# Kernel optimization log

Measured on AMD Instinct MI355X. Metric: run time of the kernel, lower is better.

## Reference

```python
import jax, jax.numpy as jnp
import numpy as np
import math

NUM_HEADS = 16
HEAD_DIM = 64
D_MODEL = NUM_HEADS * HEAD_DIM  # 1024
B, S = 4, 2048

def setup_inputs() -> dict:
    key = jax.random.key(0)
    ks = jax.random.split(key, 8)
    sd = 1.0 / math.sqrt(D_MODEL)
    return {
        "hidden_states": jax.random.normal(ks[0], (B, S, D_MODEL), jnp.float32),
        "attention_mask": jnp.zeros((B, 1, 1, S), jnp.float32),
        "Wq": jax.random.normal(ks[1], (D_MODEL, D_MODEL), jnp.float32) * sd,
        "bq": jnp.zeros((D_MODEL,), jnp.float32),
        "Wk": jax.random.normal(ks[2], (D_MODEL, D_MODEL), jnp.float32) * sd,
        "bk": jnp.zeros((D_MODEL,), jnp.float32),
        "Wv": jax.random.normal(ks[3], (D_MODEL, D_MODEL), jnp.float32) * sd,
        "bv": jnp.zeros((D_MODEL,), jnp.float32),
    }

def _split_heads(x):
    # [B, S, D] -> [B, H, S, hd]
    b, s, _ = x.shape
    return x.reshape(b, s, NUM_HEADS, HEAD_DIM).transpose(0, 2, 1, 3)

def reference(hidden_states, attention_mask, Wq, bq, Wk, bk, Wv, bv):
    # Linear projections (torch nn.Linear: x @ W.T + b)
    q = _split_heads(hidden_states @ Wq.T + bq)
    k = _split_heads(hidden_states @ Wk.T + bk)
    v = _split_heads(hidden_states @ Wv.T + bv)
    scale = 1.0 / math.sqrt(HEAD_DIM)
    # [B, H, Sq, Sk] attention scores, fully materialized as in the original
    scores = jnp.einsum("bhqd,bhkd->bhqk", q, k) * scale + attention_mask
    # relusq replacement for softmax
    probs = jnp.square(jax.nn.relu(scores))
    ctx = jnp.einsum("bhqk,bhkd->bhqd", probs, v)  # [B, H, S, hd]
    b = ctx.shape[0]
    return ctx.transpose(0, 2, 1, 3).reshape(b, -1, D_MODEL)
```

## Files before the change

### kernel.cpp

```cpp
#include <hip/hip_runtime.h>


typedef __bf16 bf16x8 __attribute__((ext_vector_type(8)));
typedef __bf16 bf16x4 __attribute__((ext_vector_type(4)));
typedef __bf16 bf16x2 __attribute__((ext_vector_type(2)));
typedef short  s16x4  __attribute__((ext_vector_type(4)));
typedef float  f32x4  __attribute__((ext_vector_type(4)));
typedef float  f32x16 __attribute__((ext_vector_type(16)));
typedef float  floatx4 __attribute__((ext_vector_type(4)));
typedef unsigned u32x2 __attribute__((ext_vector_type(2)));
typedef unsigned u32x4 __attribute__((ext_vector_type(4)));

#define MFMA16(a, b, c) __builtin_amdgcn_mfma_f32_16x16x32_bf16(a, b, c, 0, 0, 0)
#define MFMA32(a, b, c) __builtin_amdgcn_mfma_f32_32x32x16_bf16(a, b, c, 0, 0, 0)

#define WAITCNT_VM0() __builtin_amdgcn_s_waitcnt(0x0F70)
#define WAITCNT_VM6() __builtin_amdgcn_s_waitcnt(0x0F76)
#define BARRIER() __builtin_amdgcn_s_barrier()
#define SETPRIO(p) __builtin_amdgcn_s_setprio(p)

__device__ __forceinline__ void glds16(const __bf16* g, __bf16* l) {
    __builtin_amdgcn_global_load_lds(
        (const __attribute__((address_space(1))) void*)g,
        (__attribute__((address_space(3))) void*)l, 16, 0, 0);
}

__global__ __launch_bounds__(256) void convert_kernel(
    const float* __restrict__ X, const float* __restrict__ Wq,
    const float* __restrict__ Wk, const float* __restrict__ Wv,
    __bf16* __restrict__ Xb, __bf16* __restrict__ Wqb,
    __bf16* __restrict__ Wkb, __bf16* __restrict__ Wvb)
{
    int blk = blockIdx.x;
    const float* src; __bf16* dst; size_t base;
    if (blk < 4096)      { src = X;  dst = Xb;  base = (size_t)blk * 2048; }
    else if (blk < 4608) { src = Wq; dst = Wqb; base = (size_t)(blk - 4096) * 2048; }
    else if (blk < 5120) { src = Wk; dst = Wkb; base = (size_t)(blk - 4608) * 2048; }
    else                 { src = Wv; dst = Wvb; base = (size_t)(blk - 5120) * 2048; }
    size_t off = base + (size_t)threadIdx.x * 8;
    floatx4 a = *(const floatx4*)(src + off);
    floatx4 c = *(const floatx4*)(src + off + 4);
    bf16x8 o;
    o[0] = (__bf16)a[0]; o[1] = (__bf16)a[1]; o[2] = (__bf16)a[2]; o[3] = (__bf16)a[3];
    o[4] = (__bf16)c[0]; o[5] = (__bf16)c[1]; o[6] = (__bf16)c[2]; o[7] = (__bf16)c[3];
    *(bf16x8*)(dst + off) = o;
}

__global__ __launch_bounds__(512, 2) void qkv_gemm_kernel(
    const __bf16* __restrict__ Xb,
    const __bf16* __restrict__ Wqb, const __bf16* __restrict__ Wkb,
    const __bf16* __restrict__ Wvb,
    const float* __restrict__ bq, const float* __restrict__ bk,
    const float* __restrict__ bv,
    __bf16* __restrict__ qws, __bf16* __restrict__ kws, __bf16* __restrict__ vws)
{
    __shared__ __bf16 As[3][256 * 64];
    __shared__ __bf16 Bs[3][128 * 64];

    const int tid  = threadIdx.x;
    const int lane = tid & 63;
    const int wave = tid >> 6;
    const int quad = lane >> 4;
    const int l16  = lane & 15;
    const int m0   = blockIdx.y * 256;

    const int sel = blockIdx.x >> 3;
    const bool vmode = (sel == 2);
    const __bf16* Wb = (sel == 0) ? Wqb : (sel == 1) ? Wkb : Wvb;
    const float* bias = (sel == 0) ? bq : (sel == 1) ? bk : bv;
    __bf16* outp = (sel == 0) ? qws : (sel == 1) ? kws : vws;
    const int n0 = (blockIdx.x & 7) * 128;

    const int wA = vmode ? (wave & 3) * 64 : (wave >> 2) * 64;
    const int wB = vmode ? (wave >> 2) * 64 : (wave & 3) * 64;

    const int srow = lane >> 3;
    const int schk = lane & 7;

    f32x4 acc[4][4] = {};

#define QKV_STAGE_A(bb, kt, i) { \
        int rb_ = wave * 32 + (i) * 8; int r_ = rb_ + srow; \
        int c_ = schk ^ (r_ & 7); \
        glds16(Xb + (size_t)(m0 + r_) * 1024 + (kt) * 64 + c_ * 8, \
               &As[bb][rb_ * 64]); }
#define QKV_STAGE_B(bb, kt, i) { \
        int rb_ = wave * 16 + (i) * 8; int r_ = rb_ + srow; \
        int c_ = schk ^ (r_ & 7); \
        glds16(Wb + (size_t)(n0 + r_) * 1024 + (kt) * 64 + c_ * 8, \
               &Bs[bb][rb_ * 64]); }

    #pragma unroll
    for (int i = 0; i < 4; ++i) QKV_STAGE_A(0, 0, i);
    #pragma unroll
    for (int i = 0; i < 2; ++i) QKV_STAGE_B(0, 0, i);
    #pragma unroll
    for (int i = 0; i < 4; ++i) QKV_STAGE_A(1, 1, i);
    #pragma unroll
    for (int i = 0; i < 2; ++i) QKV_STAGE_B(1, 1, i);
    WAITCNT_VM6();
    BARRIER();

    for (int s = 0; s < 16; ++s) {
        const int cb  = s % 3;
        const int pb  = (s + 2) % 3;
        const int kt2 = (s + 2) & 15;
        const __bf16* Pa_ = vmode ? &As[cb][0] : &Bs[cb][0];
        const __bf16* Pb_ = vmode ? &Bs[cb][0] : &As[cb][0];

        #pragma unroll
        for (int p = 0; p < 2; ++p) {
            bf16x8 af[4], bfr[4];
            #pragma unroll
            for (int a = 0; a < 4; ++a)
                af[a] = *(const bf16x8*)&Pa_[(wA + a * 16 + l16) * 64 +
                                             (((p * 4 + quad) ^ (l16 & 7)) * 8)];
            #pragma unroll
            for (int bb = 0; bb < 4; ++bb)
                bfr[bb] = *(const bf16x8*)&Pb_[(wB + bb * 16 + l16) * 64 +
                                               (((p * 4 + quad) ^ (l16 & 7)) * 8)];
            QKV_STAGE_A(pb, kt2, 2 * p);
            QKV_STAGE_A(pb, kt2, 2 * p + 1);
            QKV_STAGE_B(pb, kt2, p);

            if (p == 1) WAITCNT_VM6();
            BARRIER();

            SETPRIO(1);
            #pragma unroll
            for (int a = 0; a < 4; ++a)
                #pragma unroll
                for (int bb = 0; bb < 4; ++bb)
                    acc[a][bb] = MFMA16(af[a], bfr[bb], acc[a][bb]);
            SETPRIO(0);
            BARRIER();
        }
    }

#undef QKV_STAGE_A
#undef QKV_STAGE_B

    if (!vmode) {
        #pragma unroll
        for (int a = 0; a < 4; ++a) {
            int n = n0 + wA + a * 16 + quad * 4;
            floatx4 bv4 = *(const floatx4*)&bias[n];
            int h = n >> 6, d0 = n & 63;
            #pragma unroll
            for (int bb = 0; bb < 4; ++bb) {
                int m = m0 + wB + bb * 16 + l16;
                int bt = m >> 11, ss = m & 2047;
                bf16x4 o;
                #pragma unroll
                for (int r = 0; r < 4; ++r)
                    o[r] = (__bf16)(acc[a][bb][r] + bv4[r]);
                *(bf16x4*)&outp[((size_t)(bt * 16 + h) * 2048 + ss) * 64 + d0] = o;
            }
        }
    } else {
        #pragma unroll
        for (int a = 0; a < 4; ++a) {
            int m = m0 + wA + a * 16 + quad * 4;
            int bt = m >> 11, s0 = m & 2047;
            #pragma unroll
            for (int bb = 0; bb < 4; ++bb) {
                int n = n0 + wB + bb * 16 + l16;
                float bvv = bias[n];
                int h = n >> 6, d = n & 63;
                bf16x4 o;
                #pragma unroll
                for (int r = 0; r < 4; ++r)
                    o[r] = (__bf16)(acc[a][bb][r] + bvv);
                *(bf16x4*)&outp[((size_t)(bt * 16 + h) * 64 + d) * 2048 + s0] = o;
            }
        }
    }
}

__global__ __launch_bounds__(512, 4) void attn_kernel(
    const __bf16* __restrict__ Q, const __bf16* __restrict__ K,
    const __bf16* __restrict__ Vt, const float* __restrict__ mask,
    float* __restrict__ out)
{
    __shared__ __bf16 Ks[2][2][64 * 64];
    __shared__ __bf16 Vs[2][2][64 * 64];
    __shared__ float  Ms[2048];

    const int tid  = threadIdx.x;
    const int lane = tid & 63;
    const int wave = tid >> 6;
    const int l32  = lane & 31;
    const int hi   = lane >> 5;
    const int bh   = blockIdx.x;
    const int b    = bh >> 4;
    const int h    = bh & 15;
    const int q0w  = blockIdx.y * 256 + wave * 32;

    const __bf16* Qb = Q  + (size_t)bh * 2048 * 64;
    const __bf16* Kb = K  + (size_t)bh * 2048 * 64;
    const __bf16* Vb = Vt + (size_t)bh * 64 * 2048;
    const float*  mb = mask + b * 2048;

    const int rb = wave * 8;
    const int sr = rb + (lane >> 3);
    const int sc = ((lane & 7) ^ (sr & 7)) * 8;

    bf16x8 aq[4];
    #pragma unroll
    for (int dk = 0; dk < 4; ++dk)
        aq[dk] = *(const bf16x8*)(Qb +
            (size_t)(q0w + l32) * 64 + dk * 16 + hi * 8);

    f32x16 co0 = {}, co1 = {};

    glds16(Kb + (size_t)sr * 64 + sc,        &Ks[0][0][rb * 64]);
    glds16(Kb + (size_t)(64 + sr) * 64 + sc, &Ks[0][1][rb * 64]);
    glds16(Vb + (size_t)sr * 2048 + sc,      &Vs[0][0][rb * 64]);
    glds16(Vb + (size_t)sr * 2048 + 64 + sc, &Vs[0][1][rb * 64]);
    glds16((const __bf16*)mb + (size_t)wave * 512 + lane * 8,
           (__bf16*)Ms + wave * 512);
    WAITCNT_VM0();
    BARRIER();

    for (int t = 0; t < 16; ++t) {
        const int kn = ((t + 1) & 15) * 128;
        const int nb = (t + 1) & 1;
        const int cb = t & 1;
        glds16(Kb + (size_t)(kn + sr) * 64 + sc,       &Ks[nb][0][rb * 64]);
        glds16(Kb + (size_t)(kn + 64 + sr) * 64 + sc,  &Ks[nb][1][rb * 64]);
        glds16(Vb + (size_t)sr * 2048 + kn + sc,       &Vs[nb][0][rb * 64]);
        glds16(Vb + (size_t)sr * 2048 + kn + 64 + sc,  &Vs[nb][1][rb * 64]);

        #pragma unroll
        for (int hf = 0; hf < 2; ++hf) {
            const __bf16* Kt = &Ks[cb][hf][0];
            const __bf16* Vtl = &Vs[cb][hf][0];
            const int k0 = t * 128 + hf * 64;

            f32x16 st0 = {}, st1 = {};
            SETPRIO(1);
            #pragma unroll
            for (int dk = 0; dk < 4; ++dk) {
                const int g = dk * 2 + hi;
                const int c0 = (g ^ (l32 & 7)) * 8;
                bf16x8 ak0 = *(const bf16x8*)&Kt[l32 * 64 + c0];
                bf16x8 ak1 = *(const bf16x8*)&Kt[(32 + l32) * 64 + c0];
                st0 = MFMA32(ak0, aq[dk], st0);
                st1 = MFMA32(ak1, aq[dk], st1);
            }
            SETPRIO(0);

            #pragma unroll
            for (int kg = 0; kg < 2; ++kg) {
                const f32x16 s = kg ? st1 : st0;
                const f32x4 zero4 = {};
                unsigned W[4][2];
                #pragma unroll
                for (int G = 0; G < 4; ++G) {
                    f32x4 v;
                    v[0] = s[G * 4 + 0]; v[1] = s[G * 4 + 1];
                    v[2] = s[G * 4 + 2]; v[3] = s[G * 4 + 3];
                    f32x4 mk = *(const f32x4*)&Ms[k0 + kg * 32 + G * 8 + hi * 4];
                    v = v * 0.125f + mk;
                    v = __builtin_elementwise_max(v, zero4);
                    v = v * v;
                    bf16x2 w0, w1;
                    w0[0] = (__bf16)v[0]; w0[1] = (__bf16)v[1];
                    w1[0] = (__bf16)v[2]; w1[1] = (__bf16)v[3];
                    W[G][0] = __builtin_bit_cast(unsigned, w0);
                    W[G][1] = __builtin_bit_cast(unsigned, w1);
                }
                u32x2 s00 = __builtin_amdgcn_permlane32_swap(W[0][0], W[1][0], false, false);
                u32x2 s01 = __builtin_amdgcn_permlane32_swap(W[0][1], W[1][1], false, false);
                u32x2 s10 = __builtin_amdgcn_permlane32_swap(W[2][0], W[3][0], false, false);
                u32x2 s11 = __builtin_amdgcn_permlane32_swap(W[2][1], W[3][1], false, false);
                u32x4 f0, f1;
                f0[0] = s00[0]; f0[1] = s01[0]; f0[2] = s00[1]; f0[3] = s01[1];
                f1[0] = s10[0]; f1[1] = s11[0]; f1[2] = s10[1]; f1[3] = s11[1];
                bf16x8 pa0 = __builtin_bit_cast(bf16x8, f0);
                bf16x8 pa1 = __builtin_bit_cast(bf16x8, f1);

                SETPRIO(1);
                #pragma unroll
                for (int dt = 0; dt < 2; ++dt) {
                    const int d = dt * 32 + l32;
                    const int ch0 = (kg * 4 + hi) ^ (d & 7);
                    const int ch1 = (kg * 4 + 2 + hi) ^ (d & 7);
                    bf16x8 vb0 = *(const bf16x8*)&Vtl[d * 64 + ch0 * 8];
                    bf16x8 vb1 = *(const bf16x8*)&Vtl[d * 64 + ch1 * 8];
                    if (dt == 0) {
                        co0 = MFMA32(pa0, vb0, co0);
                        co0 = MFMA32(pa1, vb1, co0);
                    } else {
                        co1 = MFMA32(pa0, vb0, co1);
                        co1 = MFMA32(pa1, vb1, co1);
                    }
                }
                SETPRIO(0);
            }
        }

        WAITCNT_VM0();
        BARRIER();
    }

    #pragma unroll
    for (int r = 0; r < 16; ++r) {
        int q = q0w + (r & 3) + 8 * (r >> 2) + 4 * hi;
        float* orow = &out[(((size_t)b * 2048 + q) * 16 + h) * 64];
        orow[l32]      = co0[r];
        orow[32 + l32] = co1[r];
    }
}

extern "C" void kernel_launch(void* const* d_in, const int* in_sizes, int n_in,
                              void* d_out, int out_size, void* d_ws, size_t ws_size,
                              hipStream_t stream) {
    const float* hidden = (const float*)d_in[0];
    const float* mask   = (const float*)d_in[1];
    const float* Wq     = (const float*)d_in[2];
    const float* bq     = (const float*)d_in[3];
    const float* Wk     = (const float*)d_in[4];
    const float* bk     = (const float*)d_in[5];
    const float* Wv     = (const float*)d_in[6];
    const float* bv     = (const float*)d_in[7];
    float* out = (float*)d_out;

    __bf16* qws = (__bf16*)d_ws;
    __bf16* kws = qws + (size_t)64 * 2048 * 64;
    __bf16* vws = kws + (size_t)64 * 2048 * 64;
    __bf16* Xb  = vws + (size_t)64 * 2048 * 64;
    __bf16* Wqb = Xb  + (size_t)8192 * 1024;
    __bf16* Wkb = Wqb + (size_t)1024 * 1024;
    __bf16* Wvb = Wkb + (size_t)1024 * 1024;

    convert_kernel<<<dim3(5632), dim3(256), 0, stream>>>(hidden, Wq, Wk, Wv,
                                                         Xb, Wqb, Wkb, Wvb);
    qkv_gemm_kernel<<<dim3(24, 32), dim3(512), 0, stream>>>(Xb, Wqb, Wkb, Wvb,
                                                            bq, bk, bv,
                                                            qws, kws, vws);
    attn_kernel<<<dim3(64, 8), dim3(512), 0, stream>>>(qws, kws, vws, mask, out);
}
```

Baseline: 240.9 us.

## Give each attention wave two 32-row query tiles, halving waves per block

The attention kernel now runs 4 waves of 256 threads per block, each owning 64 query rows as two 32-row groups. K and V fragments read from LDS are reused across both query groups, which halves LDS read traffic per MFMA. Each thread loads twice as many K/V/mask chunks per stage. The cost is roughly double the accumulator and fragment registers, with launch bounds relaxed to 2 blocks per SM. Fewer waves are then available to hide latency.

```diff
diff --git a/kernel.cpp b/kernel.cpp
--- a/kernel.cpp
+++ b/kernel.cpp
@@ -177,7 +177,7 @@
     }
 }
 
-__global__ __launch_bounds__(512, 4) void attn_kernel(
+__global__ __launch_bounds__(256, 2) void attn_kernel(
     const __bf16* __restrict__ Q, const __bf16* __restrict__ K,
     const __bf16* __restrict__ Vt, const float* __restrict__ mask,
     float* __restrict__ out)
@@ -194,31 +194,39 @@
     const int bh   = blockIdx.x;
     const int b    = bh >> 4;
     const int h    = bh & 15;
-    const int q0w  = blockIdx.y * 256 + wave * 32;
+    const int q0w  = blockIdx.y * 256 + wave * 64;
 
     const __bf16* Qb = Q  + (size_t)bh * 2048 * 64;
     const __bf16* Kb = K  + (size_t)bh * 2048 * 64;
     const __bf16* Vb = Vt + (size_t)bh * 64 * 2048;
     const float*  mb = mask + b * 2048;
 
-    const int rb = wave * 8;
+    const int rb = wave * 16;
     const int sr = rb + (lane >> 3);
     const int sc = ((lane & 7) ^ (sr & 7)) * 8;
 
-    bf16x8 aq[4];
-    #pragma unroll
-    for (int dk = 0; dk < 4; ++dk)
-        aq[dk] = *(const bf16x8*)(Qb +
-            (size_t)(q0w + l32) * 64 + dk * 16 + hi * 8);
-
-    f32x16 co0 = {}, co1 = {};
-
-    glds16(Kb + (size_t)sr * 64 + sc,        &Ks[0][0][rb * 64]);
-    glds16(Kb + (size_t)(64 + sr) * 64 + sc, &Ks[0][1][rb * 64]);
-    glds16(Vb + (size_t)sr * 2048 + sc,      &Vs[0][0][rb * 64]);
-    glds16(Vb + (size_t)sr * 2048 + 64 + sc, &Vs[0][1][rb * 64]);
-    glds16((const __bf16*)mb + (size_t)wave * 512 + lane * 8,
-           (__bf16*)Ms + wave * 512);
+    bf16x8 aq[2][4];
+    #pragma unroll
+    for (int qg = 0; qg < 2; ++qg)
+        #pragma unroll
+        for (int dk = 0; dk < 4; ++dk)
+            aq[qg][dk] = *(const bf16x8*)(Qb +
+                (size_t)(q0w + qg * 32 + l32) * 64 + dk * 16 + hi * 8);
+
+    f32x16 co[2][2] = {};
+
+    glds16(Kb + (size_t)sr * 64 + sc,              &Ks[0][0][rb * 64]);
+    glds16(Kb + (size_t)(sr + 8) * 64 + sc,        &Ks[0][0][(rb + 8) * 64]);
+    glds16(Kb + (size_t)(64 + sr) * 64 + sc,       &Ks[0][1][rb * 64]);
+    glds16(Kb + (size_t)(64 + sr + 8) * 64 + sc,   &Ks[0][1][(rb + 8) * 64]);
+    glds16(Vb + (size_t)sr * 2048 + sc,            &Vs[0][0][rb * 64]);
+    glds16(Vb + (size_t)(sr + 8) * 2048 + sc,      &Vs[0][0][(rb + 8) * 64]);
+    glds16(Vb + (size_t)sr * 2048 + 64 + sc,       &Vs[0][1][rb * 64]);
+    glds16(Vb + (size_t)(sr + 8) * 2048 + 64 + sc, &Vs[0][1][(rb + 8) * 64]);
+    glds16((const __bf16*)mb + (size_t)(wave * 2) * 512 + lane * 8,
+           (__bf16*)Ms + (wave * 2) * 512);
+    glds16((const __bf16*)mb + (size_t)(wave * 2 + 1) * 512 + lane * 8,
+           (__bf16*)Ms + (wave * 2 + 1) * 512);
     WAITCNT_VM0();
     BARRIER();
 
@@ -226,10 +234,14 @@
         const int kn = ((t + 1) & 15) * 128;
         const int nb = (t + 1) & 1;
         const int cb = t & 1;
-        glds16(Kb + (size_t)(kn + sr) * 64 + sc,       &Ks[nb][0][rb * 64]);
-        glds16(Kb + (size_t)(kn + 64 + sr) * 64 + sc,  &Ks[nb][1][rb * 64]);
-        glds16(Vb + (size_t)sr * 2048 + kn + sc,       &Vs[nb][0][rb * 64]);
-        glds16(Vb + (size_t)sr * 2048 + kn + 64 + sc,  &Vs[nb][1][rb * 64]);
+        glds16(Kb + (size_t)(kn + sr) * 64 + sc,            &Ks[nb][0][rb * 64]);
+        glds16(Kb + (size_t)(kn + sr + 8) * 64 + sc,        &Ks[nb][0][(rb + 8) * 64]);
+        glds16(Kb + (size_t)(kn + 64 + sr) * 64 + sc,       &Ks[nb][1][rb * 64]);
+        glds16(Kb + (size_t)(kn + 64 + sr + 8) * 64 + sc,   &Ks[nb][1][(rb + 8) * 64]);
+        glds16(Vb + (size_t)sr * 2048 + kn + sc,            &Vs[nb][0][rb * 64]);
+        glds16(Vb + (size_t)(sr + 8) * 2048 + kn + sc,      &Vs[nb][0][(rb + 8) * 64]);
+        glds16(Vb + (size_t)sr * 2048 + kn + 64 + sc,       &Vs[nb][1][rb * 64]);
+        glds16(Vb + (size_t)(sr + 8) * 2048 + kn + 64 + sc, &Vs[nb][1][(rb + 8) * 64]);
 
         #pragma unroll
         for (int hf = 0; hf < 2; ++hf) {
@@ -237,67 +249,80 @@
             const __bf16* Vtl = &Vs[cb][hf][0];
             const int k0 = t * 128 + hf * 64;
 
-            f32x16 st0 = {}, st1 = {};
+            bf16x8 akf[2][4];
+            #pragma unroll
+            for (int dk = 0; dk < 4; ++dk) {
+                const int c0 = ((dk * 2 + hi) ^ (l32 & 7)) * 8;
+                akf[0][dk] = *(const bf16x8*)&Kt[l32 * 64 + c0];
+                akf[1][dk] = *(const bf16x8*)&Kt[(32 + l32) * 64 + c0];
+            }
+            f32x16 st[2][2] = {};
             SETPRIO(1);
             #pragma unroll
-            for (int dk = 0; dk < 4; ++dk) {
-                const int g = dk * 2 + hi;
-                const int c0 = (g ^ (l32 & 7)) * 8;
-                bf16x8 ak0 = *(const bf16x8*)&Kt[l32 * 64 + c0];
-                bf16x8 ak1 = *(const bf16x8*)&Kt[(32 + l32) * 64 + c0];
-                st0 = MFMA32(ak0, aq[dk], st0);
-                st1 = MFMA32(ak1, aq[dk], st1);
-            }
+            for (int dk = 0; dk < 4; ++dk)
+                #pragma unroll
+                for (int qg = 0; qg < 2; ++qg) {
+                    st[qg][0] = MFMA32(akf[0][dk], aq[qg][dk], st[qg][0]);
+                    st[qg][1] = MFMA32(akf[1][dk], aq[qg][dk], st[qg][1]);
+                }
             SETPRIO(0);
 
+            bf16x8 paf0[2][2], paf1[2][2];
+            const f32x4 zero4 = {};
+            #pragma unroll
+            for (int qg = 0; qg < 2; ++qg)
+                #pragma unroll
+                for (int kg = 0; kg < 2; ++kg) {
+                    unsigned W[4][2];
+                    #pragma unroll
+                    for (int G = 0; G < 4; ++G) {
+                        f32x4 v;
+                        v[0] = st[qg][kg][G * 4 + 0];
+                        v[1] = st[qg][kg][G * 4 + 1];
+                        v[2] = st[qg][kg][G * 4 + 2];
+                        v[3] = st[qg][kg][G * 4 + 3];
+                        f32x4 mk = *(const f32x4*)&Ms[k0 + kg * 32 + G * 8 + hi * 4];
+                        v = v * 0.125f + mk;
+                        v = __builtin_elementwise_max(v, zero4);
+                        v = v * v;
+                        bf16x2 w0, w1;
+                        w0[0] = (__bf16)v[0]; w0[1] = (__bf16)v[1];
+                        w1[0] = (__bf16)v[2]; w1[1] = (__bf16)v[3];
+                        W[G][0] = __builtin_bit_cast(unsigned, w0);
+                        W[G][1] = __builtin_bit_cast(unsigned, w1);
+                    }
+                    u32x2 s00 = __builtin_amdgcn_permlane32_swap(W[0][0], W[1][0], false, false);
+                    u32x2 s01 = __builtin_amdgcn_permlane32_swap(W[0][1], W[1][1], false, false);
+                    u32x2 s10 = __builtin_amdgcn_permlane32_swap(W[2][0], W[3][0], false, false);
+                    u32x2 s11 = __builtin_amdgcn_permlane32_swap(W[2][1], W[3][1], false, false);
+                    u32x4 f0, f1;
+                    f0[0] = s00[0]; f0[1] = s01[0]; f0[2] = s00[1]; f0[3] = s01[1];
+                    f1[0] = s10[0]; f1[1] = s11[0]; f1[2] = s10[1]; f1[3] = s11[1];
+                    paf0[qg][kg] = __builtin_bit_cast(bf16x8, f0);
+                    paf1[qg][kg] = __builtin_bit_cast(bf16x8, f1);
+                }
+
+            SETPRIO(1);
             #pragma unroll
             for (int kg = 0; kg < 2; ++kg) {
-                const f32x16 s = kg ? st1 : st0;
-                const f32x4 zero4 = {};
-                unsigned W[4][2];
-                #pragma unroll
-                for (int G = 0; G < 4; ++G) {
-                    f32x4 v;
-                    v[0] = s[G * 4 + 0]; v[1] = s[G * 4 + 1];
-                    v[2] = s[G * 4 + 2]; v[3] = s[G * 4 + 3];
-                    f32x4 mk = *(const f32x4*)&Ms[k0 + kg * 32 + G * 8 + hi * 4];
-                    v = v * 0.125f + mk;
-                    v = __builtin_elementwise_max(v, zero4);
-                    v = v * v;
-                    bf16x2 w0, w1;
-                    w0[0] = (__bf16)v[0]; w0[1] = (__bf16)v[1];
-                    w1[0] = (__bf16)v[2]; w1[1] = (__bf16)v[3];
-                    W[G][0] = __builtin_bit_cast(unsigned, w0);
-                    W[G][1] = __builtin_bit_cast(unsigned, w1);
-                }
-                u32x2 s00 = __builtin_amdgcn_permlane32_swap(W[0][0], W[1][0], false, false);
-                u32x2 s01 = __builtin_amdgcn_permlane32_swap(W[0][1], W[1][1], false, false);
-                u32x2 s10 = __builtin_amdgcn_permlane32_swap(W[2][0], W[3][0], false, false);
-                u32x2 s11 = __builtin_amdgcn_permlane32_swap(W[2][1], W[3][1], false, false);
-                u32x4 f0, f1;
-                f0[0] = s00[0]; f0[1] = s01[0]; f0[2] = s00[1]; f0[3] = s01[1];
-                f1[0] = s10[0]; f1[1] = s11[0]; f1[2] = s10[1]; f1[3] = s11[1];
-                bf16x8 pa0 = __builtin_bit_cast(bf16x8, f0);
-                bf16x8 pa1 = __builtin_bit_cast(bf16x8, f1);
-
-                SETPRIO(1);
+                bf16x8 vb0[2], vb1[2];
                 #pragma unroll
                 for (int dt = 0; dt < 2; ++dt) {
                     const int d = dt * 32 + l32;
                     const int ch0 = (kg * 4 + hi) ^ (d & 7);
                     const int ch1 = (kg * 4 + 2 + hi) ^ (d & 7);
-                    bf16x8 vb0 = *(const bf16x8*)&Vtl[d * 64 + ch0 * 8];
-                    bf16x8 vb1 = *(const bf16x8*)&Vtl[d * 64 + ch1 * 8];
-                    if (dt == 0) {
-                        co0 = MFMA32(pa0, vb0, co0);
-                        co0 = MFMA32(pa1, vb1, co0);
-                    } else {
-                        co1 = MFMA32(pa0, vb0, co1);
-                        co1 = MFMA32(pa1, vb1, co1);
+                    vb0[dt] = *(const bf16x8*)&Vtl[d * 64 + ch0 * 8];
+                    vb1[dt] = *(const bf16x8*)&Vtl[d * 64 + ch1 * 8];
+                }
+                #pragma unroll
+                for (int qg = 0; qg < 2; ++qg)
+                    #pragma unroll
+                    for (int dt = 0; dt < 2; ++dt) {
+                        co[qg][dt] = MFMA32(paf0[qg][kg], vb0[dt], co[qg][dt]);
+                        co[qg][dt] = MFMA32(paf1[qg][kg], vb1[dt], co[qg][dt]);
                     }
-                }
-                SETPRIO(0);
             }
+            SETPRIO(0);
         }
 
         WAITCNT_VM0();
@@ -305,12 +330,14 @@
     }
 
     #pragma unroll
-    for (int r = 0; r < 16; ++r) {
-        int q = q0w + (r & 3) + 8 * (r >> 2) + 4 * hi;
-        float* orow = &out[(((size_t)b * 2048 + q) * 16 + h) * 64];
-        orow[l32]      = co0[r];
-        orow[32 + l32] = co1[r];
-    }
+    for (int qg = 0; qg < 2; ++qg)
+        #pragma unroll
+        for (int r = 0; r < 16; ++r) {
+            int q = q0w + qg * 32 + (r & 3) + 8 * (r >> 2) + 4 * hi;
+            float* orow = &out[(((size_t)b * 2048 + q) * 16 + h) * 64];
+            orow[l32]      = co[qg][0][r];
+            orow[32 + l32] = co[qg][1][r];
+        }
 }
 
 extern "C" void kernel_launch(void* const* d_in, const int* in_sizes, int n_in,
@@ -339,5 +366,5 @@
     qkv_gemm_kernel<<<dim3(24, 32), dim3(512), 0, stream>>>(Xb, Wqb, Wkb, Wvb,
                                                             bq, bk, bv,
                                                             qws, kws, vws);
-    attn_kernel<<<dim3(64, 8), dim3(512), 0, stream>>>(qws, kws, vws, mask, out);
-}
+    attn_kernel<<<dim3(64, 8), dim3(256), 0, stream>>>(qws, kws, vws, mask, out);
+}
```

Result: faster. 234.3 us (-2.7%).
